# Performance work log

Measured on AMD Instinct MI355X. Metric: run time of the kernel, lower is better.

Reference implementation:

```python
import jax, jax.numpy as jnp
import numpy as np

ALPHA = 1.702
LIMIT = 7.0


def setup_inputs() -> dict:
    E, H, D = 16, 2880, 2880
    B, S = 2, 1024
    T = B * S
    key = jax.random.key(0)
    ks = jax.random.split(key, 8)
    hidden_states = jax.random.normal(ks[0], (B, S, H), dtype=jnp.float32)
    routing_weights = jax.random.uniform(ks[1], (T, E), dtype=jnp.float32)
    scale = 0.02
    Wg = jax.random.normal(ks[2], (E, H, D), dtype=jnp.float32) * scale
    bg = jax.random.normal(ks[3], (E, D), dtype=jnp.float32) * scale
    Wu = jax.random.normal(ks[4], (E, H, D), dtype=jnp.float32) * scale
    bu = jax.random.normal(ks[5], (E, D), dtype=jnp.float32) * scale
    Wd = jax.random.normal(ks[6], (E, D, H), dtype=jnp.float32) * scale
    bd = jax.random.normal(ks[7], (E, H), dtype=jnp.float32) * scale
    return {"hidden_states": hidden_states, "routing_weights": routing_weights,
            "Wg": Wg, "bg": bg, "Wu": Wu, "bu": bu, "Wd": Wd, "bd": bd}


def reference(hidden_states, routing_weights, Wg, bg, Wu, bu, Wd, bd):
    orig_shape = hidden_states.shape
    H = Wg.shape[1]
    x = hidden_states.reshape(-1, H)  # [T, H]
    # per-expert gate/up projections: [E, T, D]
    gate = jnp.einsum('th,ehd->etd', x, Wg) + bg[:, None, :]
    gate = jnp.minimum(gate, LIMIT)
    up = jnp.einsum('th,ehd->etd', x, Wu) + bu[:, None, :]
    up = jnp.clip(up, -LIMIT, LIMIT)
    glu = gate * jax.nn.sigmoid(gate * ALPHA)
    inter = (up + 1.0) * glu  # [E, T, D]
    # down projection: [E, T, H]
    down = jnp.einsum('etd,edh->eth', inter, Wd) + bd[:, None, :]
    # routing-weighted sum over experts: [T, H]
    out = jnp.einsum('eth,te->th', down, routing_weights)
    return out.reshape(orig_shape)
```

## Files before the change

kernel.cpp:

```cpp
#include <hip/hip_runtime.h>
#include <cstdint>


#define ALPHA 1.702f
#define LIMIT 7.0f

static constexpr int E = 16;
static constexpr int H = 2880;
static constexpr int D = 2880;
static constexpr int T = 2048;
static constexpr int NKT = H / 64;

typedef float        f32x4  __attribute__((ext_vector_type(4)));
typedef short        bf16x8 __attribute__((ext_vector_type(8)));

#define MFMA_BF16(a,b,c) __builtin_amdgcn_mfma_f32_16x16x32_bf16((a),(b),(c),0,0,0)
#define SBAR()        __builtin_amdgcn_s_barrier()
#define SCHED_FENCE() __builtin_amdgcn_sched_barrier(0)

__device__ __forceinline__ unsigned short f2bf(float f){
  unsigned u = __builtin_bit_cast(unsigned, f);
  u += 0x7fffu + ((u >> 16) & 1u);
  return (unsigned short)(u >> 16);
}
__device__ __forceinline__ unsigned pack2(float a, float b){
  return (unsigned)f2bf(a) | ((unsigned)f2bf(b) << 16);
}

__device__ __forceinline__ void gload_lds16(const void* g, void* l){
  __builtin_amdgcn_global_load_lds((const __attribute__((address_space(1))) unsigned*)g,
                                   (__attribute__((address_space(3))) unsigned*)l,
                                   16, 0, 0);
}

__global__ void cvt_kernel(const float* __restrict__ in, unsigned short* __restrict__ ob, int n8){
  int i = blockIdx.x * 256 + threadIdx.x;
  if (i < n8){
    float4 a = ((const float4*)in)[2*i];
    float4 b = ((const float4*)in)[2*i+1];
    uint4 o;
    o.x = pack2(a.x, a.y); o.y = pack2(a.z, a.w);
    o.z = pack2(b.x, b.y); o.w = pack2(b.z, b.w);
    ((uint4*)ob)[i] = o;
  }
}

__global__ __launch_bounds__(256) void tcvt_kernel(
    const float* __restrict__ src, unsigned short* __restrict__ dst)
{
  __shared__ unsigned short tl[64*72];
  const int t = threadIdx.x;
  const size_t mo = (size_t)blockIdx.z * H * D;
  const int r0 = blockIdx.x * 64, c0 = blockIdx.y * 64;
  const float* s = src + mo;
  unsigned short* o = dst + mo;

  int rr = t >> 2;
  #pragma unroll
  for (int p = 0; p < 4; ++p){
    int cc = ((t & 3) + p*4) * 4;
    float4 v = *(const float4*)(s + (size_t)(r0 + rr)*D + c0 + cc);
    tl[(cc+0)*72 + rr] = f2bf(v.x);
    tl[(cc+1)*72 + rr] = f2bf(v.y);
    tl[(cc+2)*72 + rr] = f2bf(v.z);
    tl[(cc+3)*72 + rr] = f2bf(v.w);
  }
  __syncthreads();
  #pragma unroll
  for (int p = 0; p < 2; ++p){
    int task = p*256 + t;
    int cl = task >> 3, ch = task & 7;
    bf16x8 v = *(const bf16x8*)&tl[cl*72 + ch*8];
    *(bf16x8*)(o + (size_t)(c0 + cl)*H + r0 + ch*8) = v;
  }
}

__global__ __launch_bounds__(256, 2) void gateup_kernel(
    const unsigned short* __restrict__ xb,
    const unsigned short* __restrict__ wgT,
    const float* __restrict__ bg,
    const unsigned short* __restrict__ wuT,
    const float* __restrict__ bu,
    unsigned short* __restrict__ inter,
    int e0)
{
  __shared__ short As[2][128*64];
  __shared__ short Bg[2][96*64];
  __shared__ short Bu[2][96*64];

  const int t = threadIdx.x, lane = t & 63, wv = t >> 6;
  const int wm = wv >> 1, wn = wv & 1;

  int nbx = gridDim.x, nby = gridDim.y;
  int lin = blockIdx.x + nbx*(blockIdx.y + nby*blockIdx.z);
  int per = (nbx*nby*gridDim.z) >> 3;
  int id2 = (lin & 7)*per + (lin >> 3);
  int bx = id2 % nbx; int rem = id2 / nbx;
  int by = rem % nby; int bz = rem / nby;

  const int trow0 = bx * 128, ncol0 = by * 96, ez = bz, e = e0 + ez;
  const unsigned short* wg = wgT + (size_t)ez * D * H;
  const unsigned short* wu = wuT + (size_t)ez * D * H;

  f32x4 accg[4][3], accu[4][3];
  #pragma unroll
  for (int i = 0; i < 4; ++i)
    #pragma unroll
    for (int j = 0; j < 3; ++j){
      accg[i][j] = (f32x4){0.f,0.f,0.f,0.f};
      accu[i][j] = (f32x4){0.f,0.f,0.f,0.f};
    }

  auto stage = [&](int kt, int buf){
    #pragma unroll
    for (int i = 0; i < 4; ++i){
      int task = i*256 + t, row = task >> 3, ch = task & 7, sch = ch ^ (row & 7);
      gload_lds16(xb + (size_t)(trow0 + row)*H + kt*64 + sch*8, &As[buf][task*8]);
    }
    #pragma unroll
    for (int j = 0; j < 3; ++j){
      int task = j*256 + t, row = task >> 3, ch = task & 7, sch = ch ^ (row & 7);
      size_t go = (size_t)(ncol0 + row)*H + kt*64 + sch*8;
      gload_lds16(wg + go, &Bg[buf][task*8]);
      gload_lds16(wu + go, &Bu[buf][task*8]);
    }
  };

  stage(0, 0);

  for (int kt = 0; kt < NKT; ++kt){
    int cur = kt & 1, nxt = cur ^ 1;
    int ktn = (kt+1 < NKT) ? kt+1 : kt;
    stage(ktn, nxt);
    asm volatile("s_waitcnt vmcnt(10)" ::: "memory");
    SCHED_FENCE(); SBAR(); SCHED_FENCE();
    #pragma unroll
    for (int kk = 0; kk < 2; ++kk){
      bf16x8 af[4];
      #pragma unroll
      for (int mi = 0; mi < 4; ++mi){
        int row = wm*64 + mi*16 + (lane & 15);
        int pc  = (kk*4 + (lane>>4)) ^ (row & 7);
        af[mi] = *(const bf16x8*)&As[cur][row*64 + pc*8];
      }
      bf16x8 fgv[3], fuv[3];
      #pragma unroll
      for (int ni = 0; ni < 3; ++ni){
        int row = (wn*3 + ni)*16 + (lane & 15);
        int pc  = (kk*4 + (lane>>4)) ^ (row & 7);
        fgv[ni] = *(const bf16x8*)&Bg[cur][row*64 + pc*8];
        fuv[ni] = *(const bf16x8*)&Bu[cur][row*64 + pc*8];
      }
      #pragma unroll
      for (int ni = 0; ni < 3; ++ni)
        #pragma unroll
        for (int mi = 0; mi < 4; ++mi){
          accg[mi][ni] = MFMA_BF16(af[mi], fgv[ni], accg[mi][ni]);
          accu[mi][ni] = MFMA_BF16(af[mi], fuv[ni], accu[mi][ni]);
        }
    }
    SBAR();
  }
  asm volatile("s_waitcnt vmcnt(0)" ::: "memory");

  const float* bgp = bg + (size_t)e * D;
  const float* bup = bu + (size_t)e * D;
  unsigned short* ip = inter + (size_t)ez * T * D;
  #pragma unroll
  for (int ni = 0; ni < 3; ++ni){
    int d = ncol0 + wn*48 + ni*16 + (lane & 15);
    float bgv = bgp[d], buv = bup[d];
    #pragma unroll
    for (int mi = 0; mi < 4; ++mi){
      #pragma unroll
      for (int r = 0; r < 4; ++r){
        int trw = trow0 + wm*64 + mi*16 + (lane >> 4)*4 + r;
        float g = accg[mi][ni][r] + bgv;
        float u = accu[mi][ni][r] + buv;
        g = fminf(g, LIMIT);
        u = fminf(fmaxf(u, -LIMIT), LIMIT);
        float glu = g / (1.f + __expf(-ALPHA * g));
        ip[(size_t)trw * D + d] = f2bf((u + 1.f) * glu);
      }
    }
  }
}

__global__ __launch_bounds__(256, 2) void down_kernel(
    const unsigned short* __restrict__ inter,
    const unsigned short* __restrict__ wdT,
    const float* __restrict__ bd,
    const float* __restrict__ rw,
    float* __restrict__ out,
    int e0, int ec)
{
  __shared__ short As[2][128*64];
  __shared__ short Bs[2][96*64];

  const int t = threadIdx.x, lane = t & 63, wv = t >> 6;
  const int wm = wv >> 1, wn = wv & 1;

  int nbx = gridDim.x, nby = gridDim.y;
  int lin = blockIdx.x + nbx*blockIdx.y;
  int per = (nbx*nby) >> 3;
  int id2 = (lin & 7)*per + (lin >> 3);
  int bx = id2 % nbx;
  int by = id2 / nbx;

  const int trow0 = bx * 128, ncol0 = by * 96;

  f32x4 oacc[4][3];
  #pragma unroll
  for (int i = 0; i < 4; ++i)
    #pragma unroll
    for (int j = 0; j < 3; ++j) oacc[i][j] = (f32x4){0.f,0.f,0.f,0.f};

  auto stage = [&](int ee, int kt, int buf){
    const unsigned short* ap = inter + (size_t)ee * T * D;
    const unsigned short* wd = wdT + (size_t)ee * H * D;
    #pragma unroll
    for (int i = 0; i < 4; ++i){
      int task = i*256 + t, row = task >> 3, ch = task & 7, sch = ch ^ (row & 7);
      gload_lds16(ap + (size_t)(trow0 + row)*D + kt*64 + sch*8, &As[buf][task*8]);
    }
    #pragma unroll
    for (int j = 0; j < 3; ++j){
      int task = j*256 + t, row = task >> 3, ch = task & 7, sch = ch ^ (row & 7);
      gload_lds16(wd + (size_t)(ncol0 + row)*D + kt*64 + sch*8, &Bs[buf][task*8]);
    }
  };

  stage(0, 0, 0);

  int gkt = 0;
  for (int ee = 0; ee < ec; ++ee){
    const int e = e0 + ee;
    f32x4 acc[4][3];
    #pragma unroll
    for (int i = 0; i < 4; ++i)
      #pragma unroll
      for (int j = 0; j < 3; ++j) acc[i][j] = (f32x4){0.f,0.f,0.f,0.f};

    for (int kt = 0; kt < NKT; ++kt, ++gkt){
      int cur = gkt & 1, nxt = cur ^ 1;
      int eeN, ktN;
      if (kt+1 < NKT)      { eeN = ee;   ktN = kt+1; }
      else if (ee+1 < ec)  { eeN = ee+1; ktN = 0;    }
      else                 { eeN = ee;   ktN = kt;   }
      stage(eeN, ktN, nxt);
      asm volatile("s_waitcnt vmcnt(7)" ::: "memory");
      SCHED_FENCE(); SBAR(); SCHED_FENCE();
      #pragma unroll
      for (int kk = 0; kk < 2; ++kk){
        bf16x8 af[4];
        #pragma unroll
        for (int mi = 0; mi < 4; ++mi){
          int row = wm*64 + mi*16 + (lane & 15);
          int pc  = (kk*4 + (lane>>4)) ^ (row & 7);
          af[mi] = *(const bf16x8*)&As[cur][row*64 + pc*8];
        }
        bf16x8 fb[3];
        #pragma unroll
        for (int ni = 0; ni < 3; ++ni){
          int row = (wn*3 + ni)*16 + (lane & 15);
          int pc  = (kk*4 + (lane>>4)) ^ (row & 7);
          fb[ni] = *(const bf16x8*)&Bs[cur][row*64 + pc*8];
        }
        #pragma unroll
        for (int ni = 0; ni < 3; ++ni)
          #pragma unroll
          for (int mi = 0; mi < 4; ++mi)
            acc[mi][ni] = MFMA_BF16(af[mi], fb[ni], acc[mi][ni]);
      }
      SBAR();
    }

    const float* bdp = bd + (size_t)e * H;
    #pragma unroll
    for (int ni = 0; ni < 3; ++ni){
      int h = ncol0 + wn*48 + ni*16 + (lane & 15);
      float bdv = bdp[h];
      #pragma unroll
      for (int mi = 0; mi < 4; ++mi){
        #pragma unroll
        for (int r = 0; r < 4; ++r){
          int trw = trow0 + wm*64 + mi*16 + (lane >> 4)*4 + r;
          float rv = rw[trw*E + e];
          oacc[mi][ni][r] += rv * (acc[mi][ni][r] + bdv);
        }
      }
    }
  }
  asm volatile("s_waitcnt vmcnt(0)" ::: "memory");

  const int accum = (e0 != 0);
  #pragma unroll
  for (int ni = 0; ni < 3; ++ni){
    int h = ncol0 + wn*48 + ni*16 + (lane & 15);
    #pragma unroll
    for (int mi = 0; mi < 4; ++mi){
      #pragma unroll
      for (int r = 0; r < 4; ++r){
        int trw = trow0 + wm*64 + mi*16 + (lane >> 4)*4 + r;
        size_t oi = (size_t)trw * H + h;
        float v = oacc[mi][ni][r];
        if (accum) v += out[oi];
        out[oi] = v;
      }
    }
  }
}

extern "C" void kernel_launch(void* const* d_in, const int* in_sizes, int n_in,
                              void* d_out, int out_size, void* d_ws, size_t ws_size,
                              hipStream_t stream) {
  const float* hs  = (const float*)d_in[0];
  const float* rwt = (const float*)d_in[1];
  const float* Wg  = (const float*)d_in[2];
  const float* bg  = (const float*)d_in[3];
  const float* Wu  = (const float*)d_in[4];
  const float* bu  = (const float*)d_in[5];
  const float* Wd  = (const float*)d_in[6];
  const float* bd  = (const float*)d_in[7];
  float* out = (float*)d_out;

  const size_t xbytes = (size_t)T * H * 2;
  const size_t interB = (size_t)T * D * 2;
  const size_t wB     = (size_t)H * D * 2;
  const size_t perE   = interB + 2*wB;

  long long avail = (long long)ws_size - (long long)xbytes;
  int EC = (int)(avail / (long long)perE);
  if (EC < 1) EC = 1;
  if (EC > E) EC = E;

  unsigned short* xb    = (unsigned short*)d_ws;
  unsigned short* inter = (unsigned short*)((char*)d_ws + xbytes);
  unsigned short* wgT   = (unsigned short*)((char*)d_ws + xbytes + (size_t)EC*interB);
  unsigned short* wuT   = wgT + (size_t)EC * H * D;
  unsigned short* wdT   = wgT;

  cvt_kernel<<<(T*H/8 + 255)/256, 256, 0, stream>>>(hs, xb, T*H/8);

  for (int e0 = 0; e0 < E; e0 += EC){
    int ec = (E - e0 < EC) ? (E - e0) : EC;
    tcvt_kernel<<<dim3(45,45,ec), 256, 0, stream>>>(Wg + (size_t)e0*H*D, wgT);
    tcvt_kernel<<<dim3(45,45,ec), 256, 0, stream>>>(Wu + (size_t)e0*H*D, wuT);
    gateup_kernel<<<dim3(T/128, D/96, ec), 256, 0, stream>>>(xb, wgT, bg, wuT, bu, inter, e0);
    tcvt_kernel<<<dim3(45,45,ec), 256, 0, stream>>>(Wd + (size_t)e0*D*H, wdT);
    down_kernel<<<dim3(T/128, H/96), 256, 0, stream>>>(inter, wdT, bd, rwt, out, e0, ec);
  }
}
```

Baseline: 2.283 ms.

## Split down-projection over expert groups with partial outputs and a final reduce

The down kernel's expert loop is split across four groups along grid z. Each group accumulates into its own fp32 partial output buffer, and a new reduce kernel sums the four partials into the output. The N tile also grows from 96 to 192 columns, doubling the B tile in LDS and the accumulator registers. This is meant to raise parallelism in the down GEMM, which previously had only 16x30 blocks running long serial expert loops. In exchange it needs 4x T*H fp32 of extra workspace plus the reduce traffic, and the larger accumulator set adds register pressure.

```diff
diff --git a/kernel.cpp b/kernel.cpp
--- a/kernel.cpp
+++ b/kernel.cpp
@@ -10,6 +10,7 @@
 static constexpr int D = 2880;
 static constexpr int T = 2048;
 static constexpr int NKT = H / 64;
+static constexpr int NG  = 4;
 
 typedef float        f32x4  __attribute__((ext_vector_type(4)));
 typedef short        bf16x8 __attribute__((ext_vector_type(8)));
@@ -72,6 +73,17 @@
     int cl = task >> 3, ch = task & 7;
     bf16x8 v = *(const bf16x8*)&tl[cl*72 + ch*8];
     *(bf16x8*)(o + (size_t)(c0 + cl)*H + r0 + ch*8) = v;
+  }
+}
+
+__global__ void reduce_kernel(const float* __restrict__ p, float* __restrict__ out, int n4){
+  int i = blockIdx.x * 256 + threadIdx.x;
+  if (i < n4){
+    f32x4 a = ((const f32x4*)p)[i];
+    #pragma unroll
+    for (int g = 1; g < NG; ++g)
+      a += ((const f32x4*)(p + (size_t)g * T * H))[i];
+    ((f32x4*)out)[i] = a;
   }
 }
 
@@ -191,29 +203,30 @@
     const unsigned short* __restrict__ wdT,
     const float* __restrict__ bd,
     const float* __restrict__ rw,
-    float* __restrict__ out,
+    float* __restrict__ pout,
     int e0, int ec)
 {
   __shared__ short As[2][128*64];
-  __shared__ short Bs[2][96*64];
+  __shared__ short Bs[2][192*64];
 
   const int t = threadIdx.x, lane = t & 63, wv = t >> 6;
   const int wm = wv >> 1, wn = wv & 1;
 
   int nbx = gridDim.x, nby = gridDim.y;
-  int lin = blockIdx.x + nbx*blockIdx.y;
-  int per = (nbx*nby) >> 3;
+  int lin = blockIdx.x + nbx*(blockIdx.y + nby*blockIdx.z);
+  int per = (nbx*nby*gridDim.z) >> 3;
   int id2 = (lin & 7)*per + (lin >> 3);
-  int bx = id2 % nbx;
-  int by = id2 / nbx;
-
-  const int trow0 = bx * 128, ncol0 = by * 96;
-
-  f32x4 oacc[4][3];
+  int bx = id2 % nbx; int rem = id2 / nbx;
+  int by = rem % nby; int g  = rem / nby;
+
+  const int trow0 = bx * 128, ncol0 = by * 192;
+  const int ne = (ec > g) ? ((ec - 1 - g) >> 2) + 1 : 0;
+
+  f32x4 oacc[4][6];
   #pragma unroll
   for (int i = 0; i < 4; ++i)
     #pragma unroll
-    for (int j = 0; j < 3; ++j) oacc[i][j] = (f32x4){0.f,0.f,0.f,0.f};
+    for (int j = 0; j < 6; ++j) oacc[i][j] = (f32x4){0.f,0.f,0.f,0.f};
 
   auto stage = [&](int ee, int kt, int buf){
     const unsigned short* ap = inter + (size_t)ee * T * D;
@@ -224,79 +237,83 @@
       gload_lds16(ap + (size_t)(trow0 + row)*D + kt*64 + sch*8, &As[buf][task*8]);
     }
     #pragma unroll
-    for (int j = 0; j < 3; ++j){
+    for (int j = 0; j < 6; ++j){
       int task = j*256 + t, row = task >> 3, ch = task & 7, sch = ch ^ (row & 7);
       gload_lds16(wd + (size_t)(ncol0 + row)*D + kt*64 + sch*8, &Bs[buf][task*8]);
     }
   };
 
-  stage(0, 0, 0);
-
-  int gkt = 0;
-  for (int ee = 0; ee < ec; ++ee){
-    const int e = e0 + ee;
-    f32x4 acc[4][3];
-    #pragma unroll
-    for (int i = 0; i < 4; ++i)
-      #pragma unroll
-      for (int j = 0; j < 3; ++j) acc[i][j] = (f32x4){0.f,0.f,0.f,0.f};
-
-    for (int kt = 0; kt < NKT; ++kt, ++gkt){
-      int cur = gkt & 1, nxt = cur ^ 1;
-      int eeN, ktN;
-      if (kt+1 < NKT)      { eeN = ee;   ktN = kt+1; }
-      else if (ee+1 < ec)  { eeN = ee+1; ktN = 0;    }
-      else                 { eeN = ee;   ktN = kt;   }
-      stage(eeN, ktN, nxt);
-      asm volatile("s_waitcnt vmcnt(7)" ::: "memory");
-      SCHED_FENCE(); SBAR(); SCHED_FENCE();
-      #pragma unroll
-      for (int kk = 0; kk < 2; ++kk){
-        bf16x8 af[4];
+  if (ne > 0){
+    stage(g, 0, 0);
+
+    int gkt = 0;
+    for (int ei = 0; ei < ne; ++ei){
+      const int ee = g + ei*4;
+      const int e  = e0 + ee;
+      f32x4 acc[4][6];
+      #pragma unroll
+      for (int i = 0; i < 4; ++i)
+        #pragma unroll
+        for (int j = 0; j < 6; ++j) acc[i][j] = (f32x4){0.f,0.f,0.f,0.f};
+
+      for (int kt = 0; kt < NKT; ++kt, ++gkt){
+        int cur = gkt & 1, nxt = cur ^ 1;
+        int eeN, ktN;
+        if (kt+1 < NKT)      { eeN = ee;     ktN = kt+1; }
+        else if (ei+1 < ne)  { eeN = ee + 4; ktN = 0;    }
+        else                 { eeN = ee;     ktN = kt;   }
+        stage(eeN, ktN, nxt);
+        asm volatile("s_waitcnt vmcnt(10)" ::: "memory");
+        SCHED_FENCE(); SBAR(); SCHED_FENCE();
+        #pragma unroll
+        for (int kk = 0; kk < 2; ++kk){
+          bf16x8 af[4];
+          #pragma unroll
+          for (int mi = 0; mi < 4; ++mi){
+            int row = wm*64 + mi*16 + (lane & 15);
+            int pc  = (kk*4 + (lane>>4)) ^ (row & 7);
+            af[mi] = *(const bf16x8*)&As[cur][row*64 + pc*8];
+          }
+          bf16x8 fb[6];
+          #pragma unroll
+          for (int ni = 0; ni < 6; ++ni){
+            int row = wn*96 + ni*16 + (lane & 15);
+            int pc  = (kk*4 + (lane>>4)) ^ (row & 7);
+            fb[ni] = *(const bf16x8*)&Bs[cur][row*64 + pc*8];
+          }
+          #pragma unroll
+          for (int ni = 0; ni < 6; ++ni)
+            #pragma unroll
+            for (int mi = 0; mi < 4; ++mi)
+              acc[mi][ni] = MFMA_BF16(af[mi], fb[ni], acc[mi][ni]);
+        }
+        SBAR();
+      }
+
+      const float* bdp = bd + (size_t)e * H;
+      #pragma unroll
+      for (int ni = 0; ni < 6; ++ni){
+        int h = ncol0 + wn*96 + ni*16 + (lane & 15);
+        float bdv = bdp[h];
         #pragma unroll
         for (int mi = 0; mi < 4; ++mi){
-          int row = wm*64 + mi*16 + (lane & 15);
-          int pc  = (kk*4 + (lane>>4)) ^ (row & 7);
-          af[mi] = *(const bf16x8*)&As[cur][row*64 + pc*8];
+          #pragma unroll
+          for (int r = 0; r < 4; ++r){
+            int trw = trow0 + wm*64 + mi*16 + (lane >> 4)*4 + r;
+            float rv = rw[trw*E + e];
+            oacc[mi][ni][r] += rv * (acc[mi][ni][r] + bdv);
+          }
         }
-        bf16x8 fb[3];
-        #pragma unroll
-        for (int ni = 0; ni < 3; ++ni){
-          int row = (wn*3 + ni)*16 + (lane & 15);
-          int pc  = (kk*4 + (lane>>4)) ^ (row & 7);
-          fb[ni] = *(const bf16x8*)&Bs[cur][row*64 + pc*8];
-        }
-        #pragma unroll
-        for (int ni = 0; ni < 3; ++ni)
-          #pragma unroll
-          for (int mi = 0; mi < 4; ++mi)
-            acc[mi][ni] = MFMA_BF16(af[mi], fb[ni], acc[mi][ni]);
-      }
-      SBAR();
-    }
-
-    const float* bdp = bd + (size_t)e * H;
-    #pragma unroll
-    for (int ni = 0; ni < 3; ++ni){
-      int h = ncol0 + wn*48 + ni*16 + (lane & 15);
-      float bdv = bdp[h];
-      #pragma unroll
-      for (int mi = 0; mi < 4; ++mi){
-        #pragma unroll
-        for (int r = 0; r < 4; ++r){
-          int trw = trow0 + wm*64 + mi*16 + (lane >> 4)*4 + r;
-          float rv = rw[trw*E + e];
-          oacc[mi][ni][r] += rv * (acc[mi][ni][r] + bdv);
-        }
-      }
-    }
-  }
-  asm volatile("s_waitcnt vmcnt(0)" ::: "memory");
-
+      }
+    }
+    asm volatile("s_waitcnt vmcnt(0)" ::: "memory");
+  }
+
+  float* pp = pout + (size_t)g * T * H;
   const int accum = (e0 != 0);
   #pragma unroll
-  for (int ni = 0; ni < 3; ++ni){
-    int h = ncol0 + wn*48 + ni*16 + (lane & 15);
+  for (int ni = 0; ni < 6; ++ni){
+    int h = ncol0 + wn*96 + ni*16 + (lane & 15);
     #pragma unroll
     for (int mi = 0; mi < 4; ++mi){
       #pragma unroll
@@ -304,8 +321,8 @@
         int trw = trow0 + wm*64 + mi*16 + (lane >> 4)*4 + r;
         size_t oi = (size_t)trw * H + h;
         float v = oacc[mi][ni][r];
-        if (accum) v += out[oi];
-        out[oi] = v;
+        if (accum) v += pp[oi];
+        pp[oi] = v;
       }
     }
   }
@@ -325,18 +342,20 @@
   float* out = (float*)d_out;
 
   const size_t xbytes = (size_t)T * H * 2;
+  const size_t poutB  = (size_t)NG * T * H * 4;
   const size_t interB = (size_t)T * D * 2;
   const size_t wB     = (size_t)H * D * 2;
   const size_t perE   = interB + 2*wB;
 
-  long long avail = (long long)ws_size - (long long)xbytes;
+  long long avail = (long long)ws_size - (long long)(xbytes + poutB);
   int EC = (int)(avail / (long long)perE);
   if (EC < 1) EC = 1;
   if (EC > E) EC = E;
 
   unsigned short* xb    = (unsigned short*)d_ws;
-  unsigned short* inter = (unsigned short*)((char*)d_ws + xbytes);
-  unsigned short* wgT   = (unsigned short*)((char*)d_ws + xbytes + (size_t)EC*interB);
+  float*          pout  = (float*)((char*)d_ws + xbytes);
+  unsigned short* inter = (unsigned short*)((char*)d_ws + xbytes + poutB);
+  unsigned short* wgT   = (unsigned short*)((char*)d_ws + xbytes + poutB + (size_t)EC*interB);
   unsigned short* wuT   = wgT + (size_t)EC * H * D;
   unsigned short* wdT   = wgT;
 
@@ -348,6 +367,7 @@
     tcvt_kernel<<<dim3(45,45,ec), 256, 0, stream>>>(Wu + (size_t)e0*H*D, wuT);
     gateup_kernel<<<dim3(T/128, D/96, ec), 256, 0, stream>>>(xb, wgT, bg, wuT, bu, inter, e0);
     tcvt_kernel<<<dim3(45,45,ec), 256, 0, stream>>>(Wd + (size_t)e0*D*H, wdT);
-    down_kernel<<<dim3(T/128, H/96), 256, 0, stream>>>(inter, wdT, bd, rwt, out, e0, ec);
-  }
-}
+    down_kernel<<<dim3(T/128, H/192, NG), 256, 0, stream>>>(inter, wdT, bd, rwt, pout, e0, ec);
+  }
+  reduce_kernel<<<(T*H/4 + 255)/256, 256, 0, stream>>>(pout, out, T*H/4);
+}
```

New measurement: 2.265 ms. Within noise of the previous version (-0.8%).
